# Optimization experiments

Hardware: AMD Instinct MI355X
Metric: run time of the kernel (lower is better)

## Reference

```python
import jax, jax.numpy as jnp
import numpy as np

D_MODEL = 1024
ED = 2048        # d_inner = expand_factor * d_model
N = 16           # d_state
DT_RANK = 64     # ceil(d_model/16)
K = 4            # d_conv
B_SZ = 4
L = 512


def _causal_depthwise_conv(u, w, b):
    # u: [B, L, ED], w: [ED, 1, K], b: [ED]
    xc = jnp.transpose(u, (0, 2, 1))  # [B, ED, L]
    xc = jax.lax.conv_general_dilated(
        xc, w, window_strides=(1,), padding=[(K - 1, 0)],
        feature_group_count=ED, dimension_numbers=('NCH', 'OIH', 'NCH'))
    xc = xc + b[None, :, None]
    return jnp.transpose(xc, (0, 2, 1))  # [B, L, ED]


def _ssm_branch(xz_half, z, conv_w, conv_b, Wx, Wdt, b_dt, A_log, Dp):
    # xz_half, z: [B, L, ED]
    x = jax.nn.silu(_causal_depthwise_conv(xz_half, conv_w, conv_b))
    dbc = x @ Wx.T  # [B, L, dt_rank + 2N]
    delta = dbc[..., :DT_RANK]
    Bm = dbc[..., DT_RANK:DT_RANK + N]
    Cm = dbc[..., DT_RANK + N:]
    delta = jax.nn.softplus(delta @ Wdt.T + b_dt)  # [B, L, ED]
    A = -jnp.exp(A_log)  # [ED, N]
    dA = jnp.exp(delta[..., None] * A)                        # [B, L, ED, N]
    bx = (delta[..., None] * Bm[:, :, None, :]) * x[..., None]  # [B, L, ED, N]
    dA_t = jnp.transpose(dA, (1, 0, 2, 3))
    bx_t = jnp.transpose(bx, (1, 0, 2, 3))
    c_t = jnp.transpose(Cm, (1, 0, 2))  # [L, B, N]
    h0 = jnp.zeros((x.shape[0], ED, N), dtype=x.dtype)

    def step(h, inp):
        dAi, bxi, ci = inp
        h = dAi * h + bxi
        return h, jnp.einsum('ben,bn->be', h, ci)

    _, ys = jax.lax.scan(step, h0, (dA_t, bx_t, c_t))
    y = jnp.transpose(ys, (1, 0, 2)) + Dp * x  # D skip connection
    return y * jax.nn.silu(z)                  # gate


def _mamba_block(x, W_in, conv_w, conv_b, Wx, Wdt, b_dt, A_log, Dp,
                 conv_w_b, conv_b_b, Wx_b, Wdt_b, b_dt_b, A_log_b, Dp_b, W_out):
    xz = x @ W_in.T  # [B, L, 2*ED]
    xf, zf = xz[..., :ED], xz[..., ED:]
    y = _ssm_branch(xf, zf, conv_w, conv_b, Wx, Wdt, b_dt, A_log, Dp)
    xz_r = xz[:, ::-1, :]
    xb, zb = xz_r[..., :ED], xz_r[..., ED:]
    y_b = _ssm_branch(xb, zb, conv_w_b, conv_b_b, Wx_b, Wdt_b, b_dt_b, A_log_b, Dp_b)
    y = (y + y_b[:, ::-1, :]) * 0.5
    return y @ W_out.T


def setup_inputs() -> dict:
    key = jax.random.key(0)
    ks = jax.random.split(key, 20)
    s = lambda k, shp, sc: jax.random.normal(k, shp, dtype=jnp.float32) * sc
    dt = jnp.exp(jax.random.uniform(ks[15], (ED,)) * (np.log(0.1) - np.log(0.001)) + np.log(0.001))
    dt = jnp.clip(dt, 1e-4, None)
    inv_dt = dt + jnp.log(-jnp.expm1(-dt))
    A_init = jnp.log(jnp.tile(jnp.arange(1, N + 1, dtype=jnp.float32), (ED, 1)))
    return {
        'x': s(ks[0], (B_SZ, L, D_MODEL), 1.0),
        'W_in': s(ks[1], (2 * ED, D_MODEL), D_MODEL ** -0.5),
        'conv_w': s(ks[2], (ED, 1, K), K ** -0.5),
        'conv_b': s(ks[3], (ED,), 0.02),
        'Wx': s(ks[4], (DT_RANK + 2 * N, ED), ED ** -0.5),
        'Wdt': jax.random.uniform(ks[5], (ED, DT_RANK), minval=-DT_RANK ** -0.5, maxval=DT_RANK ** -0.5),
        'b_dt': inv_dt,
        'A_log': A_init,
        'Dp': jnp.ones((ED,), dtype=jnp.float32),
        'conv_w_b': s(ks[6], (ED, 1, K), K ** -0.5),
        'conv_b_b': s(ks[7], (ED,), 0.02),
        'Wx_b': s(ks[8], (DT_RANK + 2 * N, ED), ED ** -0.5),
        'Wdt_b': jax.random.uniform(ks[9], (ED, DT_RANK), minval=-DT_RANK ** -0.5, maxval=DT_RANK ** -0.5),
        'b_dt_b': inv_dt,
        'A_log_b': A_init,
        'Dp_b': jnp.ones((ED,), dtype=jnp.float32),
        'W_out': s(ks[10], (D_MODEL, ED), ED ** -0.5),
    }


def reference(x, W_in, conv_w, conv_b, Wx, Wdt, b_dt, A_log, Dp,
              conv_w_b, conv_b_b, Wx_b, Wdt_b, b_dt_b, A_log_b, Dp_b, W_out):
    return _mamba_block(x, W_in, conv_w, conv_b, Wx, Wdt, b_dt, A_log, Dp,
                        conv_w_b, conv_b_b, Wx_b, Wdt_b, b_dt_b, A_log_b, Dp_b, W_out)
```

## Files before the change

kernel.cpp:

```cpp
#include <hip/hip_runtime.h>
#include <hip/hip_bf16.h>
#include <stdint.h>

typedef unsigned short ushort_t;
typedef __attribute__((ext_vector_type(8))) short short8;
typedef __attribute__((ext_vector_type(4))) float f32x4;

__device__ __forceinline__ float b2f(ushort_t u) {
    union { uint32_t i; float f; } v; v.i = ((uint32_t)u) << 16; return v.f;
}
__device__ __forceinline__ ushort_t f2b(float f) {
    union { float f; uint32_t i; } v; v.f = f;
    uint32_t r = v.i + 0x7fff + ((v.i >> 16) & 1);
    return (ushort_t)(r >> 16);
}

__device__ __forceinline__ void ll16(const ushort_t* g, ushort_t* l) {
    __builtin_amdgcn_global_load_lds(
        (const __attribute__((address_space(1))) uint32_t*)g,
        (__attribute__((address_space(3))) uint32_t*)l, 16, 0, 0);
}

template <int CTRL>
__device__ __forceinline__ float dpp_add(float p) {
    int v = __builtin_amdgcn_update_dpp(0, __float_as_int(p), CTRL, 0xF, 0xF, true);
    return p + __int_as_float(v);
}
#define DPP_XOR1 0xB1
#define DPP_XOR2 0x4E
#define DPP_HMIR 0x141

__device__ __forceinline__ void epi_wave_f32(
    float* sw, const f32x4* accg, float* dst0, int ldc, int lane)
{
    const int quad = lane >> 4, lr = lane & 15;
#pragma unroll
    for (int j = 0; j < 4; j++)
#pragma unroll
        for (int r = 0; r < 4; r++)
            sw[(quad * 4 + r) * 64 + j * 16 + lr] = accg[j][r];
    __asm__ volatile("s_waitcnt lgkmcnt(0)" ::: "memory");
#pragma unroll
    for (int t = 0; t < 4; t++) {
        int row = t * 4 + quad;
        float4 v = *(const float4*)(&sw[row * 64 + lr * 4]);
        *(float4*)(dst0 + (size_t)row * ldc + lr * 4) = v;
    }
}

__device__ __forceinline__ void epi_wave_b16(
    float* sw, const f32x4* accg, ushort_t* dst0, int ldc, int lane)
{
    const int quad = lane >> 4, lr = lane & 15;
#pragma unroll
    for (int j = 0; j < 4; j++)
#pragma unroll
        for (int r = 0; r < 4; r++)
            sw[(quad * 4 + r) * 64 + j * 16 + lr] = accg[j][r];
    __asm__ volatile("s_waitcnt lgkmcnt(0)" ::: "memory");
#pragma unroll
    for (int t = 0; t < 4; t++) {
        int row = t * 4 + quad;
        float4 v = *(const float4*)(&sw[row * 64 + lr * 4]);
        ushort4 o; o.x = f2b(v.x); o.y = f2b(v.y); o.z = f2b(v.z); o.w = f2b(v.w);
        *(ushort4*)(dst0 + (size_t)row * ldc + lr * 4) = o;
    }
}

struct CastSeg { const float4* src; ushort4* dst; };
struct CastArgs { CastSeg seg[7]; int start[8]; };

__global__ __launch_bounds__(256) void cast_multi(CastArgs a)
{
    int g = blockIdx.x * 256 + threadIdx.x;
    if (g >= a.start[7]) return;
    int s = 0;
#pragma unroll
    for (int i = 1; i < 7; i++) s += (g >= a.start[i]);
    int i = g - a.start[s];
    float4 v = a.seg[s].src[i];
    ushort4 o;
    o.x = f2b(v.x); o.y = f2b(v.y); o.z = f2b(v.z); o.w = f2b(v.w);
    a.seg[s].dst[i] = o;
}

#define BK 32

__global__ __launch_bounds__(256) void gemm_g1(
    const ushort_t* __restrict__ A, int lda,
    const ushort_t* __restrict__ B, int ldb,
    ushort_t* __restrict__ Cout, int ldc, int Kd)
{
    __shared__ ushort_t As[128 * BK];
    __shared__ ushort_t Bs[128 * BK];
    __shared__ float sepi[4][1024];

    const int tid  = threadIdx.x;
    const int m0   = blockIdx.y * 128;
    const int n0   = blockIdx.x * 128;
    const int wv   = tid >> 6;
    const int lane = tid & 63;
    const int wm   = (wv >> 1) * 64;
    const int wn   = (wv & 1) * 64;
    const int lr   = lane & 15;
    const int quad = lane >> 4;

    f32x4 acc[4][4];
#pragma unroll
    for (int i = 0; i < 4; i++)
#pragma unroll
        for (int j = 0; j < 4; j++) acc[i][j] = f32x4{0.f, 0.f, 0.f, 0.f};

    const int srA = wv * 32 + (lane >> 2);
    const int scA = (lane & 3) * 8;

    for (int k0 = 0; k0 < Kd; k0 += BK) {
        ll16(A + (size_t)(m0 + srA) * lda + k0 + scA,      &As[wv * 1024]);
        ll16(A + (size_t)(m0 + srA + 16) * lda + k0 + scA, &As[wv * 1024 + 512]);
        ll16(B + (size_t)(n0 + srA) * ldb + k0 + scA,      &Bs[wv * 1024]);
        ll16(B + (size_t)(n0 + srA + 16) * ldb + k0 + scA, &Bs[wv * 1024 + 512]);
        __syncthreads();

        short8 af[4], bf[4];
#pragma unroll
        for (int i = 0; i < 4; i++)
            af[i] = *(const short8*)(&As[(wm + i * 16 + lr) * BK + quad * 8]);
#pragma unroll
        for (int j = 0; j < 4; j++)
            bf[j] = *(const short8*)(&Bs[(wn + j * 16 + lr) * BK + quad * 8]);
#pragma unroll
        for (int i = 0; i < 4; i++)
#pragma unroll
            for (int j = 0; j < 4; j++)
                acc[i][j] = __builtin_amdgcn_mfma_f32_16x16x32_bf16(af[i], bf[j], acc[i][j], 0, 0, 0);
        __syncthreads();
    }

#pragma unroll
    for (int g = 0; g < 4; g++)
        epi_wave_b16(sepi[wv], acc[g],
                     Cout + (size_t)(m0 + wm + g * 16) * ldc + n0 + wn, ldc, lane);
}

__global__ __launch_bounds__(256) void gemm_g4(
    const ushort_t* __restrict__ A, int lda,
    const ushort_t* __restrict__ B, int ldb,
    float* __restrict__ Cout, int ldc, int Kd)
{
    __shared__ ushort_t As[64 * BK];
    __shared__ ushort_t Bs[128 * BK];
    __shared__ float sepi[4][1024];

    const int tid  = threadIdx.x;
    const int m0   = blockIdx.y * 64;
    const int n0   = blockIdx.x * 128;
    const int wv   = tid >> 6;
    const int lane = tid & 63;
    const int wm   = (wv >> 1) * 32;
    const int wn   = (wv & 1) * 64;
    const int lr   = lane & 15;
    const int quad = lane >> 4;

    f32x4 acc[2][4];
#pragma unroll
    for (int i = 0; i < 2; i++)
#pragma unroll
        for (int j = 0; j < 4; j++) acc[i][j] = f32x4{0.f, 0.f, 0.f, 0.f};

    const int srA = wv * 16 + (lane >> 2);
    const int srB = wv * 32 + (lane >> 2);
    const int sc  = (lane & 3) * 8;

    for (int k0 = 0; k0 < Kd; k0 += BK) {
        ll16(A + (size_t)(m0 + srA) * lda + k0 + sc,      &As[wv * 512]);
        ll16(B + (size_t)(n0 + srB) * ldb + k0 + sc,      &Bs[wv * 1024]);
        ll16(B + (size_t)(n0 + srB + 16) * ldb + k0 + sc, &Bs[wv * 1024 + 512]);
        __syncthreads();

        short8 af[2], bf[4];
#pragma unroll
        for (int i = 0; i < 2; i++)
            af[i] = *(const short8*)(&As[(wm + i * 16 + lr) * BK + quad * 8]);
#pragma unroll
        for (int j = 0; j < 4; j++)
            bf[j] = *(const short8*)(&Bs[(wn + j * 16 + lr) * BK + quad * 8]);
#pragma unroll
        for (int i = 0; i < 2; i++)
#pragma unroll
            for (int j = 0; j < 4; j++)
                acc[i][j] = __builtin_amdgcn_mfma_f32_16x16x32_bf16(af[i], bf[j], acc[i][j], 0, 0, 0);
        __syncthreads();
    }

#pragma unroll
    for (int g = 0; g < 2; g++)
        epi_wave_f32(sepi[wv], acc[g],
                     Cout + (size_t)(m0 + wm + g * 16) * ldc + n0 + wn, ldc, lane);
}

__global__ __launch_bounds__(256) void gemm_g2(
    const ushort_t* __restrict__ xc, const ushort_t* __restrict__ wx,
    float* __restrict__ part)
{
    __shared__ ushort_t As[128 * BK];
    __shared__ ushort_t Bs[128 * BK];
    __shared__ float sepi[4][1024];

    const int sk = blockIdx.x, mb = blockIdx.y, br = blockIdx.z;
    const ushort_t* A = xc + (size_t)br * 2048 * 2048;
    const ushort_t* B = wx + (size_t)br * 96 * 2048;
    float* C = part + (size_t)(sk * 2 + br) * 2048 * 96;
    const int m0 = mb * 128;
    const int kb = sk * 256;

    const int tid  = threadIdx.x;
    const int wv   = tid >> 6;
    const int lane = tid & 63;
    const int wm   = (wv >> 1) * 64;
    const int wn   = (wv & 1) * 64;
    const int lr   = lane & 15;
    const int quad = lane >> 4;

    f32x4 acc[4][4];
#pragma unroll
    for (int i = 0; i < 4; i++)
#pragma unroll
        for (int j = 0; j < 4; j++) acc[i][j] = f32x4{0.f, 0.f, 0.f, 0.f};

    const int srA = wv * 32 + (lane >> 2);
    const int sc  = (lane & 3) * 8;

    for (int k0 = kb; k0 < kb + 256; k0 += BK) {
        ll16(A + (size_t)(m0 + srA) * 2048 + k0 + sc,      &As[wv * 1024]);
        ll16(A + (size_t)(m0 + srA + 16) * 2048 + k0 + sc, &As[wv * 1024 + 512]);
        ll16(B + (size_t)(srA) * 2048 + k0 + sc,           &Bs[wv * 1024]);
        ll16(B + (size_t)(srA + 16) * 2048 + k0 + sc,      &Bs[wv * 1024 + 512]);
        __syncthreads();

        short8 af[4], bf[4];
#pragma unroll
        for (int i = 0; i < 4; i++)
            af[i] = *(const short8*)(&As[(wm + i * 16 + lr) * BK + quad * 8]);
#pragma unroll
        for (int j = 0; j < 4; j++)
            bf[j] = *(const short8*)(&Bs[(wn + j * 16 + lr) * BK + quad * 8]);
#pragma unroll
        for (int i = 0; i < 4; i++)
#pragma unroll
            for (int j = 0; j < 4; j++)
                acc[i][j] = __builtin_amdgcn_mfma_f32_16x16x32_bf16(af[i], bf[j], acc[i][j], 0, 0, 0);
        __syncthreads();
    }

    float* sw = sepi[wv];
#pragma unroll
    for (int g = 0; g < 4; g++) {
#pragma unroll
        for (int j = 0; j < 4; j++)
#pragma unroll
            for (int r = 0; r < 4; r++)
                sw[(quad * 4 + r) * 64 + j * 16 + lr] = acc[g][j][r];
        __asm__ volatile("s_waitcnt lgkmcnt(0)" ::: "memory");
        int col = wn + lr * 4;
#pragma unroll
        for (int t = 0; t < 4; t++) {
            int row = t * 4 + quad;
            if (col < 96) {
                float4 v = *(const float4*)(&sw[row * 64 + lr * 4]);
                *(float4*)(C + (size_t)(m0 + wm + g * 16 + row) * 96 + col) = v;
            }
        }
    }
}

__global__ __launch_bounds__(256) void reduce_dbc(
    const float4* __restrict__ part, ushort4* __restrict__ dbc16)
{
    int g = blockIdx.x * 256 + threadIdx.x;
    const int S = 2 * 2048 * 96 / 4;
    float4 r = part[g];
#pragma unroll
    for (int i = 1; i < 8; i++) {
        float4 p = part[g + i * S];
        r.x += p.x; r.y += p.y; r.z += p.z; r.w += p.w;
    }
    ushort4 o; o.x = f2b(r.x); o.y = f2b(r.y); o.z = f2b(r.z); o.w = f2b(r.w);
    dbc16[g] = o;
}

__global__ __launch_bounds__(256) void gemm_g3(
    const ushort_t* __restrict__ dbc16, const ushort_t* __restrict__ wdt,
    ushort_t* __restrict__ delta,
    const float* __restrict__ bdt_f, const float* __restrict__ bdt_b)
{
    __shared__ ushort_t As[128 * BK];
    __shared__ ushort_t Bs[128 * BK];
    __shared__ float sepi[4][1024];

    const int br = blockIdx.z;
    const ushort_t* A = dbc16 + (size_t)br * 2048 * 96;
    const ushort_t* B = wdt + (size_t)br * 2048 * 64;
    ushort_t* C = delta + (size_t)br * 2048 * 2048;
    const float* bias = br ? bdt_b : bdt_f;

    const int tid  = threadIdx.x;
    const int m0   = blockIdx.y * 128;
    const int n0   = blockIdx.x * 128;
    const int wv   = tid >> 6;
    const int lane = tid & 63;
    const int wm   = (wv >> 1) * 64;
    const int wn   = (wv & 1) * 64;
    const int lr   = lane & 15;
    const int quad = lane >> 4;

    f32x4 acc[4][4];
#pragma unroll
    for (int i = 0; i < 4; i++)
#pragma unroll
        for (int j = 0; j < 4; j++) acc[i][j] = f32x4{0.f, 0.f, 0.f, 0.f};

    const int srA = wv * 32 + (lane >> 2);
    const int sc  = (lane & 3) * 8;

    for (int k0 = 0; k0 < 64; k0 += BK) {
        ll16(A + (size_t)(m0 + srA) * 96 + k0 + sc,       &As[wv * 1024]);
        ll16(A + (size_t)(m0 + srA + 16) * 96 + k0 + sc,  &As[wv * 1024 + 512]);
        ll16(B + (size_t)(n0 + srA) * 64 + k0 + sc,       &Bs[wv * 1024]);
        ll16(B + (size_t)(n0 + srA + 16) * 64 + k0 + sc,  &Bs[wv * 1024 + 512]);
        __syncthreads();

        short8 af[4], bf[4];
#pragma unroll
        for (int i = 0; i < 4; i++)
            af[i] = *(const short8*)(&As[(wm + i * 16 + lr) * BK + quad * 8]);
#pragma unroll
        for (int j = 0; j < 4; j++)
            bf[j] = *(const short8*)(&Bs[(wn + j * 16 + lr) * BK + quad * 8]);
#pragma unroll
        for (int i = 0; i < 4; i++)
#pragma unroll
            for (int j = 0; j < 4; j++)
                acc[i][j] = __builtin_amdgcn_mfma_f32_16x16x32_bf16(af[i], bf[j], acc[i][j], 0, 0, 0);
        __syncthreads();
    }

    float bn[4];
#pragma unroll
    for (int j = 0; j < 4; j++) bn[j] = bias[n0 + wn + j * 16 + lr];
#pragma unroll
    for (int g = 0; g < 4; g++)
#pragma unroll
        for (int j = 0; j < 4; j++)
#pragma unroll
            for (int r = 0; r < 4; r++) {
                float x = acc[g][j][r] + bn[j];
                float sp = fmaxf(x, 0.f) + __logf(1.f + __expf(-fabsf(x)));
                acc[g][j][r] = sp;
            }

#pragma unroll
    for (int g = 0; g < 4; g++)
        epi_wave_b16(sepi[wv], acc[g],
                     C + (size_t)(m0 + wm + g * 16) * 2048 + n0 + wn, 2048, lane);
}

__global__ __launch_bounds__(256) void conv_silu_kernel(
    const ushort_t* __restrict__ xz,
    const float* __restrict__ w_f, const float* __restrict__ cb_f,
    const float* __restrict__ w_b, const float* __restrict__ cb_b,
    ushort_t* __restrict__ xc16)
{
    int g = blockIdx.x * 256 + threadIdx.x;
    int e  = g & 2047;
    int t  = (g >> 11) & 511;
    int b  = (g >> 20) & 3;
    int br = g >> 22;

    const float* w  = br ? w_b  : w_f;
    const float* cb = br ? cb_b : cb_f;

    float acc = cb[e];
    float4 wv = *(const float4*)(w + e * 4);
    float wk[4] = { wv.x, wv.y, wv.z, wv.w };

#pragma unroll
    for (int k = 0; k < 4; k++) {
        int tp = t - 3 + k;
        if (tp >= 0) {
            int row = br ? (511 - tp) : tp;
            acc += wk[k] * b2f(xz[((size_t)(b * 512 + row)) * 4096 + e]);
        }
    }
    float s = acc / (1.f + __expf(-acc));
    xc16[g] = f2b(s);
}

__global__ __launch_bounds__(256) void scan_kernel(
    const ushort_t* __restrict__ delta,
    const ushort_t* __restrict__ xc,
    const ushort_t* __restrict__ dbc16,
    const ushort_t* __restrict__ xz,
    const float* __restrict__ Alog_f, const float* __restrict__ Alog_b,
    const float* __restrict__ Dp_f,   const float* __restrict__ Dp_b,
    ushort_t* __restrict__ yf, ushort_t* __restrict__ yb)
{
    const int blk = blockIdx.x;
    const int eg = blk & 63;
    const int b  = (blk >> 6) & 3;
    const int br = blk >> 8;
    const int e0 = eg * 32;

    const int tid = threadIdx.x;
    const int n2  = tid & 7;
    const int el  = tid >> 3;
    const int e   = e0 + el;

    const float* Alog = br ? Alog_b : Alog_f;
    const float* Dpp  = br ? Dp_b   : Dp_f;
    const float A0 = -__expf(Alog[e * 16 + n2]);
    const float A1 = -__expf(Alog[e * 16 + n2 + 8]);

    size_t tb = ((size_t)br * 4 + b) * 512;
    const ushort_t* dlt  = delta + tb * 2048;
    const ushort_t* xcb  = xc    + tb * 2048;
    const ushort_t* dbcb = dbc16 + tb * 96;
    ushort_t* y = (br ? yb : yf) + (size_t)b * 512 * 2048;

    __shared__ float    sd[2][32][68];
    __shared__ ushort_t sx[2][32][72];
    __shared__ ushort_t sBt[2][16][72];
    __shared__ ushort_t sCt[2][16][72];
    __shared__ float    sy[64][36];

    const int stt = tid >> 2;
    const int seg = tid & 3;
    const int swz = seg * 8;
    const int scol = stt ^ swz;

    float4 rD0 = *(const float4*)(Dpp + e0 + seg * 8);
    float4 rD1 = *(const float4*)(Dpp + e0 + seg * 8 + 4);

    uint4 rdx, rx, rbc, rx_keep;

    auto load_regs = [&](int c) {
        int t0 = c * 64;
        rdx = *(const uint4*)(dlt + (size_t)(t0 + stt) * 2048 + e0 + seg * 8);
        rx  = *(const uint4*)(xcb + (size_t)(t0 + stt) * 2048 + e0 + seg * 8);
        rbc = *(const uint4*)(dbcb + (size_t)(t0 + stt) * 96 + 64 + seg * 8);
    };
    auto write_lds = [&](int buf) {
        const uint32_t dw[4] = { rdx.x, rdx.y, rdx.z, rdx.w };
#pragma unroll
        for (int k = 0; k < 4; k++) {
            sd[buf][seg * 8 + 2 * k][scol]     = b2f((ushort_t)(dw[k] & 0xffff));
            sd[buf][seg * 8 + 2 * k + 1][scol] = b2f((ushort_t)(dw[k] >> 16));
        }
        const uint32_t xw[4] = { rx.x, rx.y, rx.z, rx.w };
#pragma unroll
        for (int k = 0; k < 4; k++) {
            sx[buf][seg * 8 + 2 * k][scol]     = (ushort_t)(xw[k] & 0xffff);
            sx[buf][seg * 8 + 2 * k + 1][scol] = (ushort_t)(xw[k] >> 16);
        }
        ushort_t* arr = (seg < 2) ? &sBt[buf][0][0] : &sCt[buf][0][0];
        const int rbase = (seg & 1) * 8;
        const uint32_t bw[4] = { rbc.x, rbc.y, rbc.z, rbc.w };
#pragma unroll
        for (int k = 0; k < 4; k++) {
            arr[(rbase + 2 * k) * 72 + scol]     = (ushort_t)(bw[k] & 0xffff);
            arr[(rbase + 2 * k + 1) * 72 + scol] = (ushort_t)(bw[k] >> 16);
        }
    };

    float h0 = 0.f, h1 = 0.f;
    const int sw = ((el >> 3) & 3) * 8;

    load_regs(0);
    write_lds(0);
    rx_keep = rx;

    for (int c = 0; c < 8; ++c) {
        if (c < 7) load_regs(c + 1);
        __syncthreads();
        const int buf = c & 1;

#pragma unroll 4
        for (int tq = 0; tq < 64; tq += 4) {
            const int tc = tq ^ sw;
            float4 dv = *(const float4*)(&sd[buf][el][tc]);
            uint2  xv = *(const uint2*)(&sx[buf][el][tc]);
            uint2 bw0 = *(const uint2*)(&sBt[buf][n2][tq]);
            uint2 bw1 = *(const uint2*)(&sBt[buf][n2 + 8][tq ^ 8]);
            uint2 cw0 = *(const uint2*)(&sCt[buf][n2][tq ^ 16]);
            uint2 cw1 = *(const uint2*)(&sCt[buf][n2 + 8][tq ^ 24]);

            float x0 = b2f((ushort_t)(xv.x & 0xffff));
            float x1 = b2f((ushort_t)(xv.x >> 16));
            float x2 = b2f((ushort_t)(xv.y & 0xffff));
            float x3 = b2f((ushort_t)(xv.y >> 16));

            float B00 = b2f((ushort_t)(bw0.x & 0xffff)), B01 = b2f((ushort_t)(bw0.x >> 16));
            float B02 = b2f((ushort_t)(bw0.y & 0xffff)), B03 = b2f((ushort_t)(bw0.y >> 16));
            float B10 = b2f((ushort_t)(bw1.x & 0xffff)), B11 = b2f((ushort_t)(bw1.x >> 16));
            float B12 = b2f((ushort_t)(bw1.y & 0xffff)), B13 = b2f((ushort_t)(bw1.y >> 16));
            float C00 = b2f((ushort_t)(cw0.x & 0xffff)), C01 = b2f((ushort_t)(cw0.x >> 16));
            float C02 = b2f((ushort_t)(cw0.y & 0xffff)), C03 = b2f((ushort_t)(cw0.y >> 16));
            float C10 = b2f((ushort_t)(cw1.x & 0xffff)), C11 = b2f((ushort_t)(cw1.x >> 16));
            float C12 = b2f((ushort_t)(cw1.y & 0xffff)), C13 = b2f((ushort_t)(cw1.y >> 16));

            float e00 = __expf(dv.x * A0), e01 = __expf(dv.y * A0);
            float e02 = __expf(dv.z * A0), e03 = __expf(dv.w * A0);
            float e10 = __expf(dv.x * A1), e11 = __expf(dv.y * A1);
            float e12 = __expf(dv.z * A1), e13 = __expf(dv.w * A1);

            float dx0 = dv.x * x0, dx1 = dv.y * x1;
            float dx2 = dv.z * x2, dx3 = dv.w * x3;

            h0 = e00 * h0 + dx0 * B00;  h1 = e10 * h1 + dx0 * B10;
            float p0 = h0 * C00 + h1 * C10;
            h0 = e01 * h0 + dx1 * B01;  h1 = e11 * h1 + dx1 * B11;
            float p1 = h0 * C01 + h1 * C11;
            h0 = e02 * h0 + dx2 * B02;  h1 = e12 * h1 + dx2 * B12;
            float p2 = h0 * C02 + h1 * C12;
            h0 = e03 * h0 + dx3 * B03;  h1 = e13 * h1 + dx3 * B13;
            float p3 = h0 * C03 + h1 * C13;

            p0 = dpp_add<DPP_XOR1>(p0); p0 = dpp_add<DPP_XOR2>(p0); p0 = dpp_add<DPP_HMIR>(p0);
            p1 = dpp_add<DPP_XOR1>(p1); p1 = dpp_add<DPP_XOR2>(p1); p1 = dpp_add<DPP_HMIR>(p1);
            p2 = dpp_add<DPP_XOR1>(p2); p2 = dpp_add<DPP_XOR2>(p2); p2 = dpp_add<DPP_HMIR>(p2);
            p3 = dpp_add<DPP_XOR1>(p3); p3 = dpp_add<DPP_XOR2>(p3); p3 = dpp_add<DPP_HMIR>(p3);

            if (n2 == 0) {
                sy[tq + 0][el] = p0;
                sy[tq + 1][el] = p1;
                sy[tq + 2][el] = p2;
                sy[tq + 3][el] = p3;
            }
        }
        __syncthreads();

        {
            int row  = c * 64 + stt;
            int orow = br ? (511 - row) : row;
            const ushort_t* zsrc = xz + ((size_t)(b * 512 + orow)) * 4096 + 2048 + e0 + seg * 8;
            uint4 zr = *(const uint4*)(zsrc);
            const uint32_t zw[4] = { zr.x, zr.y, zr.z, zr.w };
            float zv[8];
#pragma unroll
            for (int k = 0; k < 4; k++) {
                zv[2 * k]     = b2f((ushort_t)(zw[k] & 0xffff));
                zv[2 * k + 1] = b2f((ushort_t)(zw[k] >> 16));
            }
            float4 p0 = *(const float4*)(&sy[stt][seg * 8]);
            float4 p1 = *(const float4*)(&sy[stt][seg * 8 + 4]);
            const float pv[8] = { p0.x, p0.y, p0.z, p0.w, p1.x, p1.y, p1.z, p1.w };
            const uint32_t xw[4] = { rx_keep.x, rx_keep.y, rx_keep.z, rx_keep.w };
            float xvv[8];
#pragma unroll
            for (int k = 0; k < 4; k++) {
                xvv[2 * k]     = b2f((ushort_t)(xw[k] & 0xffff));
                xvv[2 * k + 1] = b2f((ushort_t)(xw[k] >> 16));
            }
            const float Dv[8] = { rD0.x, rD0.y, rD0.z, rD0.w, rD1.x, rD1.y, rD1.z, rD1.w };
            uint32_t op[4];
#pragma unroll
            for (int k = 0; k < 4; k++) {
                float ga = (pv[2 * k]     + Dv[2 * k]     * xvv[2 * k])     *
                           (zv[2 * k]     / (1.f + __expf(-zv[2 * k])));
                float gb = (pv[2 * k + 1] + Dv[2 * k + 1] * xvv[2 * k + 1]) *
                           (zv[2 * k + 1] / (1.f + __expf(-zv[2 * k + 1])));
                op[k] = (uint32_t)f2b(ga) | ((uint32_t)f2b(gb) << 16);
            }
            *(uint4*)(y + (size_t)row * 2048 + e0 + seg * 8) =
                make_uint4(op[0], op[1], op[2], op[3]);
        }

        if (c < 7) {
            write_lds((c + 1) & 1);
            rx_keep = rx;
        }
    }
}

__global__ __launch_bounds__(256) void combine_kernel(
    const uint2* __restrict__ yf, const uint2* __restrict__ yb,
    uint2* __restrict__ yc)
{
    int g = blockIdx.x * 256 + threadIdx.x;
    int e4 = g & 511;
    int t  = (g >> 9) & 511;
    int b  = g >> 18;
    uint2 a = yf[g];
    uint2 c = yb[((size_t)(b * 512 + 511 - t)) * 512 + e4];
    uint2 o;
    o.x = (uint32_t)f2b(0.5f * (b2f((ushort_t)(a.x & 0xffff)) + b2f((ushort_t)(c.x & 0xffff)))) |
          ((uint32_t)f2b(0.5f * (b2f((ushort_t)(a.x >> 16)) + b2f((ushort_t)(c.x >> 16)))) << 16);
    o.y = (uint32_t)f2b(0.5f * (b2f((ushort_t)(a.y & 0xffff)) + b2f((ushort_t)(c.y & 0xffff)))) |
          ((uint32_t)f2b(0.5f * (b2f((ushort_t)(a.y >> 16)) + b2f((ushort_t)(c.y >> 16)))) << 16);
    yc[g] = o;
}

static const size_t TT = 2048;
static const size_t OFF_XZ16  = 0;
static const size_t OFF_XC16  = OFF_XZ16  + TT*4096*2;
static const size_t OFF_DBC16 = OFF_XC16  + 2*TT*2048*2;
static const size_t OFF_DELTA = OFF_DBC16 + 2*TT*96*2;
static const size_t OFF_YF    = OFF_DELTA + 2*TT*2048*2;
static const size_t OFF_YB    = OFF_YF    + TT*2048*2;
static const size_t OFF_YC16  = OFF_YB    + TT*2048*2;
static const size_t OFF_X16   = OFF_YC16  + TT*2048*2;
static const size_t OFF_WIN16 = OFF_X16   + TT*1024*2;
static const size_t OFF_WX16  = OFF_WIN16 + 4096*1024*2;
static const size_t OFF_WDT16 = OFF_WX16  + 2*96*2048*2;
static const size_t OFF_WOUT16= OFF_WDT16 + 2*2048*64*2;
static const size_t OFF_PART  = OFF_WOUT16+ 1024*2048*2;

extern "C" void kernel_launch(void* const* d_in, const int* in_sizes, int n_in,
                              void* d_out, int out_size, void* d_ws, size_t ws_size,
                              hipStream_t stream) {
    const float* x       = (const float*)d_in[0];
    const float* W_in    = (const float*)d_in[1];
    const float* conv_w  = (const float*)d_in[2];
    const float* conv_b  = (const float*)d_in[3];
    const float* Wx      = (const float*)d_in[4];
    const float* Wdt     = (const float*)d_in[5];
    const float* b_dt    = (const float*)d_in[6];
    const float* A_log   = (const float*)d_in[7];
    const float* Dp      = (const float*)d_in[8];
    const float* conv_w_b= (const float*)d_in[9];
    const float* conv_b_b= (const float*)d_in[10];
    const float* Wx_b    = (const float*)d_in[11];
    const float* Wdt_b   = (const float*)d_in[12];
    const float* b_dt_b  = (const float*)d_in[13];
    const float* A_log_b = (const float*)d_in[14];
    const float* Dp_b    = (const float*)d_in[15];
    const float* W_out   = (const float*)d_in[16];
    float* out = (float*)d_out;

    char* ws = (char*)d_ws;
    ushort_t* xz16  = (ushort_t*)(ws + OFF_XZ16);
    ushort_t* xc16  = (ushort_t*)(ws + OFF_XC16);
    ushort_t* dbc16 = (ushort_t*)(ws + OFF_DBC16);
    ushort_t* delta = (ushort_t*)(ws + OFF_DELTA);
    ushort_t* yf    = (ushort_t*)(ws + OFF_YF);
    ushort_t* yb    = (ushort_t*)(ws + OFF_YB);
    ushort_t* yc16  = (ushort_t*)(ws + OFF_YC16);
    ushort_t* x16   = (ushort_t*)(ws + OFF_X16);
    ushort_t* win16 = (ushort_t*)(ws + OFF_WIN16);
    ushort_t* wx16  = (ushort_t*)(ws + OFF_WX16);
    ushort_t* wdt16 = (ushort_t*)(ws + OFF_WDT16);
    ushort_t* wout16= (ushort_t*)(ws + OFF_WOUT16);
    float*    part  = (float*)(ws + OFF_PART);

    dim3 blk(256);

    CastArgs ca;
    const int n4s[7] = {524288, 1048576, 49152, 49152, 32768, 32768, 524288};
    ca.seg[0] = { (const float4*)x,     (ushort4*)x16 };
    ca.seg[1] = { (const float4*)W_in,  (ushort4*)win16 };
    ca.seg[2] = { (const float4*)Wx,    (ushort4*)wx16 };
    ca.seg[3] = { (const float4*)Wx_b,  (ushort4*)(wx16 + 96 * 2048) };
    ca.seg[4] = { (const float4*)Wdt,   (ushort4*)wdt16 };
    ca.seg[5] = { (const float4*)Wdt_b, (ushort4*)(wdt16 + 2048 * 64) };
    ca.seg[6] = { (const float4*)W_out, (ushort4*)wout16 };
    ca.start[0] = 0;
    for (int i = 0; i < 7; i++) ca.start[i + 1] = ca.start[i] + n4s[i];
    cast_multi<<<(ca.start[7] + 255) / 256, blk, 0, stream>>>(ca);

    gemm_g1<<<dim3(32, 16), blk, 0, stream>>>(x16, 1024, win16, 1024, xz16, 4096, 1024);

    conv_silu_kernel<<<32768, blk, 0, stream>>>(xz16, conv_w, conv_b, conv_w_b, conv_b_b, xc16);

    gemm_g2<<<dim3(8, 16, 2), blk, 0, stream>>>(xc16, wx16, part);
    reduce_dbc<<<384, blk, 0, stream>>>((const float4*)part, (ushort4*)dbc16);

    gemm_g3<<<dim3(16, 16, 2), blk, 0, stream>>>(dbc16, wdt16, delta, b_dt, b_dt_b);

    scan_kernel<<<512, blk, 0, stream>>>(delta, xc16, dbc16, xz16, A_log, A_log_b, Dp, Dp_b, yf, yb);

    combine_kernel<<<4096, blk, 0, stream>>>((const uint2*)yf, (const uint2*)yb, (uint2*)yc16);

    gemm_g4<<<dim3(8, 32), blk, 0, stream>>>(yc16, 2048, wout16, 2048, out, 1024, 2048);
}
```

Before: 287.8 us.

## Defer scan epilogue by one chunk, prefetch z, use exp2 and fp32 B/C

```diff
diff --git a/kernel.cpp b/kernel.cpp
--- a/kernel.cpp
+++ b/kernel.cpp
@@ -14,6 +14,12 @@
     uint32_t r = v.i + 0x7fff + ((v.i >> 16) & 1);
     return (ushort_t)(r >> 16);
 }
+
+#if __has_builtin(__builtin_amdgcn_exp2f)
+#define EXP2(x) __builtin_amdgcn_exp2f(x)
+#else
+#define EXP2(x) __expf((x) * 0.69314718056f)
+#endif
 
 __device__ __forceinline__ void ll16(const ushort_t* g, ushort_t* l) {
     __builtin_amdgcn_global_load_lds(
@@ -417,8 +423,8 @@
 
     const float* Alog = br ? Alog_b : Alog_f;
     const float* Dpp  = br ? Dp_b   : Dp_f;
-    const float A0 = -__expf(Alog[e * 16 + n2]);
-    const float A1 = -__expf(Alog[e * 16 + n2 + 8]);
+    const float A0 = -__expf(Alog[e * 16 + n2]) * 1.44269504f;
+    const float A1 = -__expf(Alog[e * 16 + n2 + 8]) * 1.44269504f;
 
     size_t tb = ((size_t)br * 4 + b) * 512;
     const ushort_t* dlt  = delta + tb * 2048;
@@ -428,9 +434,9 @@
 
     __shared__ float    sd[2][32][68];
     __shared__ ushort_t sx[2][32][72];
-    __shared__ ushort_t sBt[2][16][72];
-    __shared__ ushort_t sCt[2][16][72];
-    __shared__ float    sy[64][36];
+    __shared__ float    sB[2][16][68];
+    __shared__ float    sC[2][16][68];
+    __shared__ float    sy[2][64][36];
 
     const int stt = tid >> 2;
     const int seg = tid & 3;
@@ -440,13 +446,16 @@
     float4 rD0 = *(const float4*)(Dpp + e0 + seg * 8);
     float4 rD1 = *(const float4*)(Dpp + e0 + seg * 8 + 4);
 
-    uint4 rdx, rx, rbc, rx_keep;
+    uint4 rdx, rx, rbc, rz;
+    uint4 rx_c, rx_f, rz_c, rz_f;
 
     auto load_regs = [&](int c) {
         int t0 = c * 64;
         rdx = *(const uint4*)(dlt + (size_t)(t0 + stt) * 2048 + e0 + seg * 8);
         rx  = *(const uint4*)(xcb + (size_t)(t0 + stt) * 2048 + e0 + seg * 8);
         rbc = *(const uint4*)(dbcb + (size_t)(t0 + stt) * 96 + 64 + seg * 8);
+        int orow = br ? (511 - (t0 + stt)) : (t0 + stt);
+        rz  = *(const uint4*)(xz + ((size_t)(b * 512 + orow)) * 4096 + 2048 + e0 + seg * 8);
     };
     auto write_lds = [&](int buf) {
         const uint32_t dw[4] = { rdx.x, rdx.y, rdx.z, rdx.w };
@@ -461,14 +470,47 @@
             sx[buf][seg * 8 + 2 * k][scol]     = (ushort_t)(xw[k] & 0xffff);
             sx[buf][seg * 8 + 2 * k + 1][scol] = (ushort_t)(xw[k] >> 16);
         }
-        ushort_t* arr = (seg < 2) ? &sBt[buf][0][0] : &sCt[buf][0][0];
+        float* arr = (seg < 2) ? &sB[buf][0][0] : &sC[buf][0][0];
         const int rbase = (seg & 1) * 8;
         const uint32_t bw[4] = { rbc.x, rbc.y, rbc.z, rbc.w };
 #pragma unroll
         for (int k = 0; k < 4; k++) {
-            arr[(rbase + 2 * k) * 72 + scol]     = (ushort_t)(bw[k] & 0xffff);
-            arr[(rbase + 2 * k + 1) * 72 + scol] = (ushort_t)(bw[k] >> 16);
-        }
+            arr[(rbase + 2 * k) * 68 + scol]     = b2f((ushort_t)(bw[k] & 0xffff));
+            arr[(rbase + 2 * k + 1) * 68 + scol] = b2f((ushort_t)(bw[k] >> 16));
+        }
+    };
+    auto flush = [&](int cm1) {
+        const int bufm1 = cm1 & 1;
+        int row = cm1 * 64 + stt;
+        const uint32_t zw[4] = { rz_f.x, rz_f.y, rz_f.z, rz_f.w };
+        float zv[8];
+#pragma unroll
+        for (int k = 0; k < 4; k++) {
+            zv[2 * k]     = b2f((ushort_t)(zw[k] & 0xffff));
+            zv[2 * k + 1] = b2f((ushort_t)(zw[k] >> 16));
+        }
+        float4 p0 = *(const float4*)(&sy[bufm1][stt][seg * 8]);
+        float4 p1 = *(const float4*)(&sy[bufm1][stt][seg * 8 + 4]);
+        const float pv[8] = { p0.x, p0.y, p0.z, p0.w, p1.x, p1.y, p1.z, p1.w };
+        const uint32_t xw[4] = { rx_f.x, rx_f.y, rx_f.z, rx_f.w };
+        float xvv[8];
+#pragma unroll
+        for (int k = 0; k < 4; k++) {
+            xvv[2 * k]     = b2f((ushort_t)(xw[k] & 0xffff));
+            xvv[2 * k + 1] = b2f((ushort_t)(xw[k] >> 16));
+        }
+        const float Dv[8] = { rD0.x, rD0.y, rD0.z, rD0.w, rD1.x, rD1.y, rD1.z, rD1.w };
+        uint32_t op[4];
+#pragma unroll
+        for (int k = 0; k < 4; k++) {
+            float ga = (pv[2 * k]     + Dv[2 * k]     * xvv[2 * k])     *
+                       (zv[2 * k]     / (1.f + __expf(-zv[2 * k])));
+            float gb = (pv[2 * k + 1] + Dv[2 * k + 1] * xvv[2 * k + 1]) *
+                       (zv[2 * k + 1] / (1.f + __expf(-zv[2 * k + 1])));
+            op[k] = (uint32_t)f2b(ga) | ((uint32_t)f2b(gb) << 16);
+        }
+        *(uint4*)(y + (size_t)row * 2048 + e0 + seg * 8) =
+            make_uint4(op[0], op[1], op[2], op[3]);
     };
 
     float h0 = 0.f, h1 = 0.f;
@@ -476,7 +518,7 @@
 
     load_regs(0);
     write_lds(0);
-    rx_keep = rx;
+    rx_c = rx; rz_c = rz;
 
     for (int c = 0; c < 8; ++c) {
         if (c < 7) load_regs(c + 1);
@@ -488,41 +530,32 @@
             const int tc = tq ^ sw;
             float4 dv = *(const float4*)(&sd[buf][el][tc]);
             uint2  xv = *(const uint2*)(&sx[buf][el][tc]);
-            uint2 bw0 = *(const uint2*)(&sBt[buf][n2][tq]);
-            uint2 bw1 = *(const uint2*)(&sBt[buf][n2 + 8][tq ^ 8]);
-            uint2 cw0 = *(const uint2*)(&sCt[buf][n2][tq ^ 16]);
-            uint2 cw1 = *(const uint2*)(&sCt[buf][n2 + 8][tq ^ 24]);
+            float4 B0 = *(const float4*)(&sB[buf][n2][tq]);
+            float4 B1 = *(const float4*)(&sB[buf][n2 + 8][tq ^ 8]);
+            float4 C0 = *(const float4*)(&sC[buf][n2][tq ^ 16]);
+            float4 C1 = *(const float4*)(&sC[buf][n2 + 8][tq ^ 24]);
 
             float x0 = b2f((ushort_t)(xv.x & 0xffff));
             float x1 = b2f((ushort_t)(xv.x >> 16));
             float x2 = b2f((ushort_t)(xv.y & 0xffff));
             float x3 = b2f((ushort_t)(xv.y >> 16));
 
-            float B00 = b2f((ushort_t)(bw0.x & 0xffff)), B01 = b2f((ushort_t)(bw0.x >> 16));
-            float B02 = b2f((ushort_t)(bw0.y & 0xffff)), B03 = b2f((ushort_t)(bw0.y >> 16));
-            float B10 = b2f((ushort_t)(bw1.x & 0xffff)), B11 = b2f((ushort_t)(bw1.x >> 16));
-            float B12 = b2f((ushort_t)(bw1.y & 0xffff)), B13 = b2f((ushort_t)(bw1.y >> 16));
-            float C00 = b2f((ushort_t)(cw0.x & 0xffff)), C01 = b2f((ushort_t)(cw0.x >> 16));
-            float C02 = b2f((ushort_t)(cw0.y & 0xffff)), C03 = b2f((ushort_t)(cw0.y >> 16));
-            float C10 = b2f((ushort_t)(cw1.x & 0xffff)), C11 = b2f((ushort_t)(cw1.x >> 16));
-            float C12 = b2f((ushort_t)(cw1.y & 0xffff)), C13 = b2f((ushort_t)(cw1.y >> 16));
-
-            float e00 = __expf(dv.x * A0), e01 = __expf(dv.y * A0);
-            float e02 = __expf(dv.z * A0), e03 = __expf(dv.w * A0);
-            float e10 = __expf(dv.x * A1), e11 = __expf(dv.y * A1);
-            float e12 = __expf(dv.z * A1), e13 = __expf(dv.w * A1);
+            float e00 = EXP2(dv.x * A0), e01 = EXP2(dv.y * A0);
+            float e02 = EXP2(dv.z * A0), e03 = EXP2(dv.w * A0);
+            float e10 = EXP2(dv.x * A1), e11 = EXP2(dv.y * A1);
+            float e12 = EXP2(dv.z * A1), e13 = EXP2(dv.w * A1);
 
             float dx0 = dv.x * x0, dx1 = dv.y * x1;
             float dx2 = dv.z * x2, dx3 = dv.w * x3;
 
-            h0 = e00 * h0 + dx0 * B00;  h1 = e10 * h1 + dx0 * B10;
-            float p0 = h0 * C00 + h1 * C10;
-            h0 = e01 * h0 + dx1 * B01;  h1 = e11 * h1 + dx1 * B11;
-            float p1 = h0 * C01 + h1 * C11;
-            h0 = e02 * h0 + dx2 * B02;  h1 = e12 * h1 + dx2 * B12;
-            float p2 = h0 * C02 + h1 * C12;
-            h0 = e03 * h0 + dx3 * B03;  h1 = e13 * h1 + dx3 * B13;
-            float p3 = h0 * C03 + h1 * C13;
+            h0 = e00 * h0 + dx0 * B0.x;  h1 = e10 * h1 + dx0 * B1.x;
+            float p0 = h0 * C0.x + h1 * C1.x;
+            h0 = e01 * h0 + dx1 * B0.y;  h1 = e11 * h1 + dx1 * B1.y;
+            float p1 = h0 * C0.y + h1 * C1.y;
+            h0 = e02 * h0 + dx2 * B0.z;  h1 = e12 * h1 + dx2 * B1.z;
+            float p2 = h0 * C0.z + h1 * C1.z;
+            h0 = e03 * h0 + dx3 * B0.w;  h1 = e13 * h1 + dx3 * B1.w;
+            float p3 = h0 * C0.w + h1 * C1.w;
 
             p0 = dpp_add<DPP_XOR1>(p0); p0 = dpp_add<DPP_XOR2>(p0); p0 = dpp_add<DPP_HMIR>(p0);
             p1 = dpp_add<DPP_XOR1>(p1); p1 = dpp_add<DPP_XOR2>(p1); p1 = dpp_add<DPP_HMIR>(p1);
@@ -530,55 +563,25 @@
             p3 = dpp_add<DPP_XOR1>(p3); p3 = dpp_add<DPP_XOR2>(p3); p3 = dpp_add<DPP_HMIR>(p3);
 
             if (n2 == 0) {
-                sy[tq + 0][el] = p0;
-                sy[tq + 1][el] = p1;
-                sy[tq + 2][el] = p2;
-                sy[tq + 3][el] = p3;
+                sy[buf][tq + 0][el] = p0;
+                sy[buf][tq + 1][el] = p1;
+                sy[buf][tq + 2][el] = p2;
+                sy[buf][tq + 3][el] = p3;
             }
         }
-        __syncthreads();
-
-        {
-            int row  = c * 64 + stt;
-            int orow = br ? (511 - row) : row;
-            const ushort_t* zsrc = xz + ((size_t)(b * 512 + orow)) * 4096 + 2048 + e0 + seg * 8;
-            uint4 zr = *(const uint4*)(zsrc);
-            const uint32_t zw[4] = { zr.x, zr.y, zr.z, zr.w };
-            float zv[8];
-#pragma unroll
-            for (int k = 0; k < 4; k++) {
-                zv[2 * k]     = b2f((ushort_t)(zw[k] & 0xffff));
-                zv[2 * k + 1] = b2f((ushort_t)(zw[k] >> 16));
-            }
-            float4 p0 = *(const float4*)(&sy[stt][seg * 8]);
-            float4 p1 = *(const float4*)(&sy[stt][seg * 8 + 4]);
-            const float pv[8] = { p0.x, p0.y, p0.z, p0.w, p1.x, p1.y, p1.z, p1.w };
-            const uint32_t xw[4] = { rx_keep.x, rx_keep.y, rx_keep.z, rx_keep.w };
-            float xvv[8];
-#pragma unroll
-            for (int k = 0; k < 4; k++) {
-                xvv[2 * k]     = b2f((ushort_t)(xw[k] & 0xffff));
-                xvv[2 * k + 1] = b2f((ushort_t)(xw[k] >> 16));
-            }
-            const float Dv[8] = { rD0.x, rD0.y, rD0.z, rD0.w, rD1.x, rD1.y, rD1.z, rD1.w };
-            uint32_t op[4];
-#pragma unroll
-            for (int k = 0; k < 4; k++) {
-                float ga = (pv[2 * k]     + Dv[2 * k]     * xvv[2 * k])     *
-                           (zv[2 * k]     / (1.f + __expf(-zv[2 * k])));
-                float gb = (pv[2 * k + 1] + Dv[2 * k + 1] * xvv[2 * k + 1]) *
-                           (zv[2 * k + 1] / (1.f + __expf(-zv[2 * k + 1])));
-                op[k] = (uint32_t)f2b(ga) | ((uint32_t)f2b(gb) << 16);
-            }
-            *(uint4*)(y + (size_t)row * 2048 + e0 + seg * 8) =
-                make_uint4(op[0], op[1], op[2], op[3]);
-        }
+
+        if (c > 0) flush(c - 1);
 
         if (c < 7) {
             write_lds((c + 1) & 1);
-            rx_keep = rx;
-        }
-    }
+            rx_f = rx_c; rz_f = rz_c;
+            rx_c = rx;   rz_c = rz;
+        } else {
+            rx_f = rx_c; rz_f = rz_c;
+        }
+    }
+    __syncthreads();
+    flush(7);
 }
 
 __global__ __launch_bounds__(256) void combine_kernel(
```

New measurement: 281.9 us. -2.1%, faster.
